# Kernel tuning notes

Hardware: AMD Instinct MI355X
Metric: run time of the kernel (lower is better)

## Reference

```python
import jax, jax.numpy as jnp
from jax import lax
import numpy as np

INPUT = 42
HIDDEN = 64
OUT = 2


def setup_inputs() -> dict:
    key = jax.random.key(0)
    ks = jax.random.split(key, 7)
    T, B = 2048, 512
    s_ih = 1.0 / np.sqrt(HIDDEN)
    return {
        "x": jax.random.normal(ks[0], (T, B, INPUT), dtype=jnp.float32),
        "W_ih": jax.random.uniform(ks[1], (4 * HIDDEN, INPUT), jnp.float32, -s_ih, s_ih),
        "W_hh": jax.random.uniform(ks[2], (4 * HIDDEN, HIDDEN), jnp.float32, -s_ih, s_ih),
        "b_ih": jax.random.uniform(ks[3], (4 * HIDDEN,), jnp.float32, -s_ih, s_ih),
        "b_hh": jax.random.uniform(ks[4], (4 * HIDDEN,), jnp.float32, -s_ih, s_ih),
        "W_out": jax.random.uniform(ks[5], (OUT, HIDDEN), jnp.float32, -s_ih, s_ih),
        "b_out": jax.random.uniform(ks[6], (OUT,), jnp.float32, -s_ih, s_ih),
    }


def reference(x, W_ih, W_hh, b_ih, b_hh, W_out, b_out):
    # x: (T, B, 42); PyTorch LSTM gate order: i, f, g, o
    B = x.shape[1]
    h0 = jnp.zeros((B, HIDDEN), x.dtype)
    c0 = jnp.zeros((B, HIDDEN), x.dtype)
    # Precompute input projections for all timesteps in one GEMM.
    x_proj = jnp.einsum('tbi,gi->tbg', x, W_ih) + b_ih + b_hh  # (T, B, 4H)

    def step(carry, xp):
        h, c = carry
        gates = xp + h @ W_hh.T  # (B, 4H)
        i, f, g, o = jnp.split(gates, 4, axis=-1)
        c = jax.nn.sigmoid(f) * c + jax.nn.sigmoid(i) * jnp.tanh(g)
        h = jax.nn.sigmoid(o) * jnp.tanh(c)
        return (h, c), h

    _, lstm_out = lax.scan(step, (h0, c0), x_proj)  # (T, B, H)
    # Faithful to original: lstm_out[:, -1, :] -> last BATCH element, all timesteps
    return lstm_out[:, -1, :] @ W_out.T + b_out  # (T, 2)
```

## Files before the change

kernel.cpp:

```cpp
#include <hip/hip_runtime.h>
#include <hip/hip_bf16.h>


#define T_STEPS 2048
#define BATCH   512
#define NIN     42
#define NH      64
#define NG      256
#define CH      16
#define NCHUNK  (T_STEPS / CH)
#define XT      16

#define LOG2E  1.44269504f
#define TWOL2E 2.88539008f

#if __has_builtin(__builtin_amdgcn_exp2f)
#define EXP2F __builtin_amdgcn_exp2f
#else
#define EXP2F exp2f
#endif

typedef float v2f __attribute__((ext_vector_type(2)));

__global__ __launch_bounds__(256) void xproj_kernel(
    const float* __restrict__ x, const float* __restrict__ W_ih,
    const float* __restrict__ b_ih, const float* __restrict__ b_hh,
    float* __restrict__ xp)
{
    const int g  = threadIdx.x;
    const int t0 = blockIdx.x * XT;
    __shared__ float ws[NG * NIN];
    __shared__ float xs[XT][NIN];
    for (int i = threadIdx.x; i < NG * NIN; i += 256) ws[i] = W_ih[i];
    for (int i = threadIdx.x; i < XT * NIN; i += 256) {
        int tt = i / NIN, j = i % NIN;
        xs[tt][j] = x[((size_t)(t0 + tt) * BATCH + (BATCH - 1)) * NIN + j];
    }
    const float bias = b_ih[g] + b_hh[g];
    const float sc = ((g >> 6) == 2) ? (2.f * LOG2E) : (-LOG2E);
    __syncthreads();
    const float* wr = &ws[g * NIN];
    for (int tt = 0; tt < XT; ++tt) {
        float s = bias;
#pragma unroll
        for (int i = 0; i < NIN; ++i) s += wr[i] * xs[tt][i];
        xp[(size_t)(t0 + tt) * NG + g] = s * sc;
    }
}

__device__ __forceinline__ void wg_barrier_lgkm() {
    asm volatile("s_waitcnt lgkmcnt(0)\n\ts_barrier" ::: "memory");
}

__device__ __forceinline__ void pin2(v2f& v) {
    asm volatile("" : "+v"(v));
}

template <int CTRL>
__device__ __forceinline__ float dpp_mov(float v) {
    return __int_as_float(
        __builtin_amdgcn_mov_dpp(__float_as_int(v), CTRL, 0xF, 0xF, true));
}

__device__ __forceinline__ v2f fma2(v2f a, v2f b, v2f c) {
    return __builtin_elementwise_fma(a, b, c);
}

__global__ void
__attribute__((amdgpu_flat_work_group_size(256, 256), amdgpu_waves_per_eu(1, 1)))
lstm_scan_kernel(
    const float* __restrict__ W_hh, const float* __restrict__ xp,
    float* __restrict__ hout)
{
    const int lane = threadIdx.x;
    const int kc   = lane & 3;
    const int u    = lane >> 2;

    __shared__ __align__(16) float hbuf[2][NH];
    if (lane < NH) { hbuf[0][lane] = 0.f; hbuf[1][lane] = 0.f; }

    const bool istanh = (kc == 2);
    const float gA = istanh ? -2.f : ((kc == 0) ? TWOL2E : 1.f);
    const float gB = istanh ? 1.f : 0.f;

    const int g0i = 0 ^ kc, g1i = 1 ^ kc, g2i = 2 ^ kc, g3i = 3 ^ kc;
    const float f0 = LOG2E * ((g0i == 2) ? 2.f : -1.f);
    const float f1 = LOG2E * ((g1i == 2) ? 2.f : -1.f);
    const float f2 = LOG2E * ((g2i == 2) ? 2.f : -1.f);
    const float f3 = LOG2E * ((g3i == 2) ? 2.f : -1.f);
    const v2f SC0 = {f0, f0}, SC1 = {f1, f1}, SC2 = {f2, f2}, SC3 = {f3, f3};

    const v2f* W0 = (const v2f*)(W_hh + ((size_t)g0i * NH + u) * NH + kc * 16);
    const v2f* W1 = (const v2f*)(W_hh + ((size_t)g1i * NH + u) * NH + kc * 16);
    const v2f* W2 = (const v2f*)(W_hh + ((size_t)g2i * NH + u) * NH + kc * 16);
    const v2f* W3 = (const v2f*)(W_hh + ((size_t)g3i * NH + u) * NH + kc * 16);
    v2f w0a=W0[0]*SC0, w0b=W0[1]*SC0, w0c=W0[2]*SC0, w0d=W0[3]*SC0,
        w0e=W0[4]*SC0, w0f=W0[5]*SC0, w0g=W0[6]*SC0, w0h=W0[7]*SC0;
    v2f w1a=W1[0]*SC1, w1b=W1[1]*SC1, w1c=W1[2]*SC1, w1d=W1[3]*SC1,
        w1e=W1[4]*SC1, w1f=W1[5]*SC1, w1g=W1[6]*SC1, w1h=W1[7]*SC1;
    v2f w2a=W2[0]*SC2, w2b=W2[1]*SC2, w2c=W2[2]*SC2, w2d=W2[3]*SC2,
        w2e=W2[4]*SC2, w2f=W2[5]*SC2, w2g=W2[6]*SC2, w2h=W2[7]*SC2;
    v2f w3a=W3[0]*SC3, w3b=W3[1]*SC3, w3c=W3[2]*SC3, w3d=W3[3]*SC3,
        w3e=W3[4]*SC3, w3f=W3[5]*SC3, w3g=W3[6]*SC3, w3h=W3[7]*SC3;
    pin2(w0a); pin2(w0b); pin2(w0c); pin2(w0d); pin2(w0e); pin2(w0f); pin2(w0g); pin2(w0h);
    pin2(w1a); pin2(w1b); pin2(w1c); pin2(w1d); pin2(w1e); pin2(w1f); pin2(w1g); pin2(w1h);
    pin2(w2a); pin2(w2b); pin2(w2c); pin2(w2d); pin2(w2e); pin2(w2f); pin2(w2g); pin2(w2h);
    pin2(w3a); pin2(w3b); pin2(w3c); pin2(w3d); pin2(w3e); pin2(w3f); pin2(w3g); pin2(w3h);

    float C = 0.f;
    const int seed_off = kc * NH + u;
    float* __restrict__ hp = hout + u;

    float xq[CH];
#pragma unroll
    for (int tt = 0; tt < CH; ++tt) xq[tt] = xp[tt * NG + seed_off];

    wg_barrier_lgkm();

    for (int ch = 0; ch < NCHUNK; ++ch) {
        float xn[CH];
        if (ch + 1 < NCHUNK) {
#pragma unroll
            for (int tt = 0; tt < CH; ++tt)
                xn[tt] = xp[(size_t)(ch + 1) * (CH * NG) + tt * NG + seed_off];
        }

#pragma unroll
        for (int tt = 0; tt < CH; ++tt) {
            const int p = tt & 1;
            const float4* hb = (const float4*)hbuf[p];
            float4 hv0 = hb[kc * 4 + 0];
            float4 hv1 = hb[kc * 4 + 1];
            float4 hv2 = hb[kc * 4 + 2];
            float4 hv3 = hb[kc * 4 + 3];
            v2f h0 = {hv0.x, hv0.y}, h1 = {hv0.z, hv0.w};
            v2f h2 = {hv1.x, hv1.y}, h3 = {hv1.z, hv1.w};
            v2f h4 = {hv2.x, hv2.y}, h5 = {hv2.z, hv2.w};
            v2f h6 = {hv3.x, hv3.y}, h7 = {hv3.z, hv3.w};

            v2f a0 = {xq[tt], 0.f};
            v2f a1 = {0.f, 0.f}, a2 = {0.f, 0.f}, a3 = {0.f, 0.f};

            a0 = fma2(w0a, h0, a0); a0 = fma2(w0b, h1, a0);
            a0 = fma2(w0c, h2, a0); a0 = fma2(w0d, h3, a0);
            a0 = fma2(w0e, h4, a0); a0 = fma2(w0f, h5, a0);
            a0 = fma2(w0g, h6, a0); a0 = fma2(w0h, h7, a0);
            a1 = fma2(w1a, h0, a1); a1 = fma2(w1b, h1, a1);
            a1 = fma2(w1c, h2, a1); a1 = fma2(w1d, h3, a1);
            a1 = fma2(w1e, h4, a1); a1 = fma2(w1f, h5, a1);
            a1 = fma2(w1g, h6, a1); a1 = fma2(w1h, h7, a1);
            a2 = fma2(w2a, h0, a2); a2 = fma2(w2b, h1, a2);
            a2 = fma2(w2c, h2, a2); a2 = fma2(w2d, h3, a2);
            a2 = fma2(w2e, h4, a2); a2 = fma2(w2f, h5, a2);
            a2 = fma2(w2g, h6, a2); a2 = fma2(w2h, h7, a2);
            a3 = fma2(w3a, h0, a3); a3 = fma2(w3b, h1, a3);
            a3 = fma2(w3c, h2, a3); a3 = fma2(w3d, h3, a3);
            a3 = fma2(w3e, h4, a3); a3 = fma2(w3f, h5, a3);
            a3 = fma2(w3g, h6, a3); a3 = fma2(w3h, h7, a3);

            float p0 = a0.x + a0.y;
            float p1 = a1.x + a1.y;
            float p2 = a2.x + a2.y;
            float p3 = a3.x + a3.y;

            float r0 = p0 + dpp_mov<0xB1>(p1);
            float r1 = p2 + dpp_mov<0xB1>(p3);
            float s  = r0 + dpp_mov<0x4E>(r1);

            float e = EXP2F(s);
            float r = __builtin_amdgcn_rcpf(1.f + e);
            float v = __builtin_fmaf(gA, r, gB);

            float w  = dpp_mov<0xB1>(v);
            float g0 = dpp_mov<0x4E>(v);
            float oo = dpp_mov<0x1B>(v);

            float t2  = v * g0;
            float p2o = -2.f * oo;
            C = __builtin_fmaf(w, C, t2);
            float e2 = EXP2F(C);
            float rr = __builtin_amdgcn_rcpf(1.f + e2);
            float hn = __builtin_fmaf(p2o, rr, oo);

            if (kc == 0) {
                hbuf[1 - p][u] = hn;
                hp[(size_t)(ch * CH + tt) * NH] = hn;
            }
            wg_barrier_lgkm();
        }

#pragma unroll
        for (int tt = 0; tt < CH; ++tt) xq[tt] = xn[tt];
    }
}

__global__ __launch_bounds__(256) void outproj_kernel(
    const float* __restrict__ hout, const float* __restrict__ W_out,
    const float* __restrict__ b_out, float* __restrict__ out)
{
    int idx = blockIdx.x * blockDim.x + threadIdx.x;
    if (idx >= T_STEPS * 2) return;
    int t = idx >> 1, o = idx & 1;
    const float* hr = hout + (size_t)t * NH;
    const float* wr = W_out + o * NH;
    float s = b_out[o];
#pragma unroll
    for (int j = 0; j < NH; ++j) s += hr[j] * wr[j];
    out[t * 2 + o] = s;
}

extern "C" void kernel_launch(void* const* d_in, const int* in_sizes, int n_in,
                              void* d_out, int out_size, void* d_ws, size_t ws_size,
                              hipStream_t stream) {
    const float* x     = (const float*)d_in[0];
    const float* W_ih  = (const float*)d_in[1];
    const float* W_hh  = (const float*)d_in[2];
    const float* b_ih  = (const float*)d_in[3];
    const float* b_hh  = (const float*)d_in[4];
    const float* W_out = (const float*)d_in[5];
    const float* b_out = (const float*)d_in[6];
    float* out = (float*)d_out;

    float* xp   = (float*)d_ws;
    float* hout = xp + (size_t)T_STEPS * NG;

    xproj_kernel<<<T_STEPS / XT, 256, 0, stream>>>(x, W_ih, b_ih, b_hh, xp);
    lstm_scan_kernel<<<1, 256, 0, stream>>>(W_hh, xp, hout);
    outproj_kernel<<<(T_STEPS * 2 + 255) / 256, 256, 0, stream>>>(hout, W_out, b_out, out);
}
```

Before: 722.5 us.

## Give each lane a full gate dot product and prefetch own-wave hidden chunk before barrier

```diff
diff --git a/kernel.cpp b/kernel.cpp
--- a/kernel.cpp
+++ b/kernel.cpp
@@ -48,10 +48,6 @@
     }
 }
 
-__device__ __forceinline__ void wg_barrier_lgkm() {
-    asm volatile("s_waitcnt lgkmcnt(0)\n\ts_barrier" ::: "memory");
-}
-
 __device__ __forceinline__ void pin2(v2f& v) {
     asm volatile("" : "+v"(v));
 }
@@ -75,37 +71,32 @@
     const int lane = threadIdx.x;
     const int kc   = lane & 3;
     const int u    = lane >> 2;
+    const int wv   = lane >> 6;
 
     __shared__ __align__(16) float hbuf[2][NH];
-    if (lane < NH) { hbuf[0][lane] = 0.f; hbuf[1][lane] = 0.f; }
+    if (lane < 2 * NH) ((float*)hbuf)[lane] = 0.f;
 
     const bool istanh = (kc == 2);
     const float gA = istanh ? -2.f : ((kc == 0) ? TWOL2E : 1.f);
     const float gB = istanh ? 1.f : 0.f;
-
-    const int g0i = 0 ^ kc, g1i = 1 ^ kc, g2i = 2 ^ kc, g3i = 3 ^ kc;
-    const float f0 = LOG2E * ((g0i == 2) ? 2.f : -1.f);
-    const float f1 = LOG2E * ((g1i == 2) ? 2.f : -1.f);
-    const float f2 = LOG2E * ((g2i == 2) ? 2.f : -1.f);
-    const float f3 = LOG2E * ((g3i == 2) ? 2.f : -1.f);
-    const v2f SC0 = {f0, f0}, SC1 = {f1, f1}, SC2 = {f2, f2}, SC3 = {f3, f3};
-
-    const v2f* W0 = (const v2f*)(W_hh + ((size_t)g0i * NH + u) * NH + kc * 16);
-    const v2f* W1 = (const v2f*)(W_hh + ((size_t)g1i * NH + u) * NH + kc * 16);
-    const v2f* W2 = (const v2f*)(W_hh + ((size_t)g2i * NH + u) * NH + kc * 16);
-    const v2f* W3 = (const v2f*)(W_hh + ((size_t)g3i * NH + u) * NH + kc * 16);
-    v2f w0a=W0[0]*SC0, w0b=W0[1]*SC0, w0c=W0[2]*SC0, w0d=W0[3]*SC0,
-        w0e=W0[4]*SC0, w0f=W0[5]*SC0, w0g=W0[6]*SC0, w0h=W0[7]*SC0;
-    v2f w1a=W1[0]*SC1, w1b=W1[1]*SC1, w1c=W1[2]*SC1, w1d=W1[3]*SC1,
-        w1e=W1[4]*SC1, w1f=W1[5]*SC1, w1g=W1[6]*SC1, w1h=W1[7]*SC1;
-    v2f w2a=W2[0]*SC2, w2b=W2[1]*SC2, w2c=W2[2]*SC2, w2d=W2[3]*SC2,
-        w2e=W2[4]*SC2, w2f=W2[5]*SC2, w2g=W2[6]*SC2, w2h=W2[7]*SC2;
-    v2f w3a=W3[0]*SC3, w3b=W3[1]*SC3, w3c=W3[2]*SC3, w3d=W3[3]*SC3,
-        w3e=W3[4]*SC3, w3f=W3[5]*SC3, w3g=W3[6]*SC3, w3h=W3[7]*SC3;
-    pin2(w0a); pin2(w0b); pin2(w0c); pin2(w0d); pin2(w0e); pin2(w0f); pin2(w0g); pin2(w0h);
-    pin2(w1a); pin2(w1b); pin2(w1c); pin2(w1d); pin2(w1e); pin2(w1f); pin2(w1g); pin2(w1h);
-    pin2(w2a); pin2(w2b); pin2(w2c); pin2(w2d); pin2(w2e); pin2(w2f); pin2(w2g); pin2(w2h);
-    pin2(w3a); pin2(w3b); pin2(w3c); pin2(w3d); pin2(w3e); pin2(w3f); pin2(w3g); pin2(w3h);
+    const float sc = istanh ? (2.f * LOG2E) : (-LOG2E);
+
+    v2f wr[32];
+    {
+        const v2f* W = (const v2f*)(W_hh + ((size_t)kc * NH + u) * NH);
+#pragma unroll
+        for (int m = 0; m < 4; ++m) {
+            const int c = (wv + m) & 3;
+#pragma unroll
+            for (int j = 0; j < 8; ++j) {
+                v2f t = W[c * 8 + j];
+                t.x *= sc; t.y *= sc;
+                wr[m * 8 + j] = t;
+            }
+        }
+#pragma unroll
+        for (int j = 0; j < 32; ++j) pin2(wr[j]);
+    }
 
     float C = 0.f;
     const int seed_off = kc * NH + u;
@@ -115,7 +106,18 @@
 #pragma unroll
     for (int tt = 0; tt < CH; ++tt) xq[tt] = xp[tt * NG + seed_off];
 
-    wg_barrier_lgkm();
+    const int coo = wv * 4;
+    const int co1 = ((wv + 1) & 3) * 4;
+    const int co2 = ((wv + 2) & 3) * 4;
+    const int co3 = ((wv + 3) & 3) * 4;
+
+    asm volatile("s_waitcnt lgkmcnt(0)" ::: "memory");
+    __builtin_amdgcn_s_barrier();
+    float4 o0, o1, o2, o3;
+    {
+        const float4* hb = (const float4*)hbuf[0] + coo;
+        o0 = hb[0]; o1 = hb[1]; o2 = hb[2]; o3 = hb[3];
+    }
 
     for (int ch = 0; ch < NCHUNK; ++ch) {
         float xn[CH];
@@ -129,43 +131,34 @@
         for (int tt = 0; tt < CH; ++tt) {
             const int p = tt & 1;
             const float4* hb = (const float4*)hbuf[p];
-            float4 hv0 = hb[kc * 4 + 0];
-            float4 hv1 = hb[kc * 4 + 1];
-            float4 hv2 = hb[kc * 4 + 2];
-            float4 hv3 = hb[kc * 4 + 3];
-            v2f h0 = {hv0.x, hv0.y}, h1 = {hv0.z, hv0.w};
-            v2f h2 = {hv1.x, hv1.y}, h3 = {hv1.z, hv1.w};
-            v2f h4 = {hv2.x, hv2.y}, h5 = {hv2.z, hv2.w};
-            v2f h6 = {hv3.x, hv3.y}, h7 = {hv3.z, hv3.w};
-
-            v2f a0 = {xq[tt], 0.f};
-            v2f a1 = {0.f, 0.f}, a2 = {0.f, 0.f}, a3 = {0.f, 0.f};
-
-            a0 = fma2(w0a, h0, a0); a0 = fma2(w0b, h1, a0);
-            a0 = fma2(w0c, h2, a0); a0 = fma2(w0d, h3, a0);
-            a0 = fma2(w0e, h4, a0); a0 = fma2(w0f, h5, a0);
-            a0 = fma2(w0g, h6, a0); a0 = fma2(w0h, h7, a0);
-            a1 = fma2(w1a, h0, a1); a1 = fma2(w1b, h1, a1);
-            a1 = fma2(w1c, h2, a1); a1 = fma2(w1d, h3, a1);
-            a1 = fma2(w1e, h4, a1); a1 = fma2(w1f, h5, a1);
-            a1 = fma2(w1g, h6, a1); a1 = fma2(w1h, h7, a1);
-            a2 = fma2(w2a, h0, a2); a2 = fma2(w2b, h1, a2);
-            a2 = fma2(w2c, h2, a2); a2 = fma2(w2d, h3, a2);
-            a2 = fma2(w2e, h4, a2); a2 = fma2(w2f, h5, a2);
-            a2 = fma2(w2g, h6, a2); a2 = fma2(w2h, h7, a2);
-            a3 = fma2(w3a, h0, a3); a3 = fma2(w3b, h1, a3);
-            a3 = fma2(w3c, h2, a3); a3 = fma2(w3d, h3, a3);
-            a3 = fma2(w3e, h4, a3); a3 = fma2(w3f, h5, a3);
-            a3 = fma2(w3g, h6, a3); a3 = fma2(w3h, h7, a3);
-
-            float p0 = a0.x + a0.y;
-            float p1 = a1.x + a1.y;
-            float p2 = a2.x + a2.y;
-            float p3 = a3.x + a3.y;
-
-            float r0 = p0 + dpp_mov<0xB1>(p1);
-            float r1 = p2 + dpp_mov<0xB1>(p3);
-            float s  = r0 + dpp_mov<0x4E>(r1);
+            float4 x10 = hb[co1 + 0], x11 = hb[co1 + 1],
+                   x12 = hb[co1 + 2], x13 = hb[co1 + 3];
+            float4 x20 = hb[co2 + 0], x21 = hb[co2 + 1],
+                   x22 = hb[co2 + 2], x23 = hb[co2 + 3];
+            float4 x30 = hb[co3 + 0], x31 = hb[co3 + 1],
+                   x32 = hb[co3 + 2], x33 = hb[co3 + 3];
+
+            v2f a0 = {xq[tt], 0.f}, a1 = {0.f, 0.f}, a2 = {0.f, 0.f},
+                a3 = {0.f, 0.f}, a4 = {0.f, 0.f}, a5 = {0.f, 0.f},
+                a6 = {0.f, 0.f}, a7 = {0.f, 0.f};
+#define FQ(F0, F1, F2, F3, B)                                                   \
+    a0 = fma2(wr[B + 0], (v2f){F0.x, F0.y}, a0);                                \
+    a1 = fma2(wr[B + 1], (v2f){F0.z, F0.w}, a1);                                \
+    a2 = fma2(wr[B + 2], (v2f){F1.x, F1.y}, a2);                                \
+    a3 = fma2(wr[B + 3], (v2f){F1.z, F1.w}, a3);                                \
+    a4 = fma2(wr[B + 4], (v2f){F2.x, F2.y}, a4);                                \
+    a5 = fma2(wr[B + 5], (v2f){F2.z, F2.w}, a5);                                \
+    a6 = fma2(wr[B + 6], (v2f){F3.x, F3.y}, a6);                                \
+    a7 = fma2(wr[B + 7], (v2f){F3.z, F3.w}, a7);
+            FQ(o0, o1, o2, o3, 0)
+            FQ(x10, x11, x12, x13, 8)
+            FQ(x20, x21, x22, x23, 16)
+            FQ(x30, x31, x32, x33, 24)
+#undef FQ
+            v2f t0 = a0 + a1, t1 = a2 + a3, t2v = a4 + a5, t3 = a6 + a7;
+            v2f u0v = t0 + t1, u1v = t2v + t3;
+            v2f z = u0v + u1v;
+            float s = z.x + z.y;
 
             float e = EXP2F(s);
             float r = __builtin_amdgcn_rcpf(1.f + e);
@@ -186,7 +179,14 @@
                 hbuf[1 - p][u] = hn;
                 hp[(size_t)(ch * CH + tt) * NH] = hn;
             }
-            wg_barrier_lgkm();
+            asm volatile("s_waitcnt lgkmcnt(0)" ::: "memory");
+            __builtin_amdgcn_sched_barrier(0);
+            {
+                const float4* hbn = (const float4*)hbuf[1 - p] + coo;
+                o0 = hbn[0]; o1 = hbn[1]; o2 = hbn[2]; o3 = hbn[3];
+            }
+            __builtin_amdgcn_sched_barrier(0);
+            __builtin_amdgcn_s_barrier();
         }
 
 #pragma unroll
```

Measured after the change: 860.5 us. 1.19x slower.
